# Kernel optimization log

Hardware: AMD Instinct MI355X
Metric: run time of the kernel (lower is better)

The kernel has to match this reference:

```python
import jax, jax.numpy as jnp
import numpy as np

B, S, D = 2, 2048, 1024
H, KV, HD = 16, 4, 64          # heads, kv heads, head_dim = D//H
I, E, K = 3584, 4, 2            # ffn intermediate, routed experts, top_k
WIN = 512                       # sliding window
EPS = 1e-5
THETA = 1000000.0
LIMIT = 7.0                     # swiglu clamp
NREP = H // KV
NEG = -1e30

def _rms(x, w):
    return x * jax.lax.rsqrt(jnp.mean(x * x, axis=-1, keepdims=True) + EPS) * w

def _rot_half(x):
    h = x.shape[-1] // 2
    return jnp.concatenate([-x[..., h:], x[..., :h]], axis=-1)

def _ffn(x, gw, uw, dw):
    g = jnp.minimum(x @ gw.T, LIMIT)
    u = jnp.clip(x @ uw.T, -LIMIT, LIMIT)
    return (jax.nn.silu(g) * u) @ dw.T

def setup_inputs():
    key = jax.random.key(0)
    ks = jax.random.split(key, 16)
    # rotary embeddings [S, HD]
    inv = 1.0 / (THETA ** (jnp.arange(0, HD, 2, dtype=jnp.float32) / HD))
    freqs = jnp.outer(jnp.arange(S, dtype=jnp.float32), inv)
    emb = jnp.concatenate([freqs, freqs], axis=-1)
    s = 0.02
    return dict(
        x=jax.random.normal(ks[0], (B, S, D), jnp.float32),
        cos=jnp.cos(emb), sin=jnp.sin(emb),
        attn_norm_w=jnp.ones((D,), jnp.float32),
        post_norm_w=jnp.ones((D,), jnp.float32),
        q_norm_w=jnp.ones((HD,), jnp.float32),
        k_norm_w=jnp.ones((HD,), jnp.float32),
        wq=jax.random.normal(ks[1], (H * HD, D), jnp.float32) * s,
        wk=jax.random.normal(ks[2], (KV * HD, D), jnp.float32) * s,
        wv=jax.random.normal(ks[3], (KV * HD, D), jnp.float32) * s,
        wo=jax.random.normal(ks[4], (D, H * HD), jnp.float32) * s,
        sinks=jax.random.normal(ks[5], (H,), jnp.float32),
        gate_w=jax.random.normal(ks[6], (E, D), jnp.float32) * s,
        eg_w=jax.random.normal(ks[7], (E, I, D), jnp.float32) * s,
        eu_w=jax.random.normal(ks[8], (E, I, D), jnp.float32) * s,
        ed_w=jax.random.normal(ks[9], (E, D, I), jnp.float32) * s,
        sg_w=jax.random.normal(ks[10], (I, D), jnp.float32) * s,
        su_w=jax.random.normal(ks[11], (I, D), jnp.float32) * s,
        sd_w=jax.random.normal(ks[12], (D, I), jnp.float32) * s,
    )

def _forward(x, cos, sin, attn_norm_w, wq, wk, wv, wo, q_norm_w, k_norm_w,
             sinks, post_norm_w, gate_w, eg_w, eu_w, ed_w, sg_w, su_w, sd_w):
    # ---- attention sublayer ----
    hin = _rms(x, attn_norm_w)
    q = (hin @ wq.T).reshape(B, S, H, HD)
    k = (hin @ wk.T).reshape(B, S, KV, HD)
    v = (hin @ wv.T).reshape(B, S, KV, HD)
    q = _rms(q, q_norm_w)
    k = _rms(k, k_norm_w)
    c, sn = cos[None, :, None, :], sin[None, :, None, :]
    q = q * c + _rot_half(q) * sn
    k = k * c + _rot_half(k) * sn
    k = jnp.repeat(k, NREP, axis=2)  # GQA -> [B,S,H,HD]
    v = jnp.repeat(v, NREP, axis=2)
    scores = jnp.einsum('bihd,bjhd->bhij', q, k) / np.sqrt(HD).astype(np.float32)
    idx = jnp.arange(S)
    allowed = (idx[:, None] >= idx[None, :]) & (idx[None, :] > idx[:, None] - WIN)
    scores = jnp.where(allowed[None, None], scores, NEG)
    sink = jnp.broadcast_to(sinks.reshape(1, H, 1, 1), (B, H, S, 1))
    ext = jnp.concatenate([scores, sink], axis=-1)           # [B,H,S,S+1]
    w = jax.nn.softmax(ext.astype(jnp.float32), axis=-1)[..., :-1].astype(x.dtype)
    attn = jnp.einsum('bhij,bjhd->bihd', w, v).reshape(B, S, H * HD) @ wo.T
    h1 = x + attn
    # ---- MoE FFN sublayer ----
    m = _rms(h1, post_norm_w).reshape(-1, D)                 # [T,D]
    T = m.shape[0]
    gs = jax.nn.softmax(m @ gate_w.T, axis=-1)               # [T,E]
    tw, ti = jax.lax.top_k(gs, K)
    tw = tw / (jnp.sum(tw, axis=-1, keepdims=True) + 1e-20)  # norm_topk_prob
    wd = jnp.zeros((T, E), m.dtype).at[jnp.arange(T)[:, None], ti].add(tw)
    g = jnp.minimum(jnp.einsum('td,eid->tei', m, eg_w), LIMIT)
    u = jnp.clip(jnp.einsum('td,eid->tei', m, eu_w), -LIMIT, LIMIT)
    eo = jnp.einsum('tei,edi->ted', jax.nn.silu(g) * u, ed_w)
    y = jnp.einsum('ted,te->td', eo, wd) + _ffn(m, sg_w, su_w, sd_w)
    return h1 + y.reshape(B, S, D)

def reference(x, cos, sin, attn_norm_w, post_norm_w, q_norm_w, k_norm_w,
              wq, wk, wv, wo, sinks, gate_w, eg_w, eu_w, ed_w, sg_w, su_w, sd_w):
    return _forward(x, cos, sin, attn_norm_w, wq, wk, wv, wo, q_norm_w, k_norm_w,
                    sinks, post_norm_w, gate_w, eg_w, eu_w, ed_w, sg_w, su_w, sd_w)
```

## Files before the change

### kernel.cpp

```cpp
#include <hip/hip_runtime.h>
#include <cstdint>
#include <cstddef>

#define S_LEN 2048
#define BATCH 2
#define DMODEL 1024
#define NH 16
#define NKV 4
#define HDIM 64
#define NTOK 4096
#define IDIM 3584
#define NEXP 4
#define WINSZ 512
#define EPSV 1e-5f
#define LIMV 7.0f
#define CATMAX 13056

typedef unsigned short u16;
typedef unsigned int u32;
typedef __bf16 bf16x8 __attribute__((ext_vector_type(8)));
typedef float f32x4 __attribute__((ext_vector_type(4)));
typedef u32 u32x4 __attribute__((ext_vector_type(4)));
typedef u16 u16x4 __attribute__((ext_vector_type(4)));

__device__ __forceinline__ u16 f2b(float f) {
  union { float f; u32 u; } v; v.f = f;
  return (u16)((v.u + 0x7fffu + ((v.u >> 16) & 1u)) >> 16);
}
__device__ __forceinline__ float b2f(u16 h) {
  union { u32 u; float f; } v; v.u = ((u32)h) << 16; return v.f;
}
__device__ __forceinline__ float wave_sum(float x) {
#pragma unroll
  for (int o = 32; o > 0; o >>= 1) x += __shfl_xor(x, o);
  return x;
}
__device__ __forceinline__ void gld16(const void* g, void* l) {
  __builtin_amdgcn_global_load_lds(
      (const __attribute__((address_space(1))) u32*)g,
      (__attribute__((address_space(3))) u32*)l, 16, 0, 0);
}
__device__ __forceinline__ int xcd_swz(int id, int nwg) {
  int q = nwg >> 3, rr = nwg & 7;
  int xcd = id & 7, j = id >> 3;
  return (xcd < rr ? xcd * (q + 1) : rr * (q + 1) + (xcd - rr) * q) + j;
}

__global__ void k_init(int* cnt) {
  if (threadIdx.x < NEXP) cnt[threadIdx.x] = 0;
}

struct CvtArgs {
  const float* src[10];
  u16* dh[10];
  u16* dl[10];
  int n4[10];
};
__global__ __launch_bounds__(256) void k_convert(CvtArgs a) {
  int ai = blockIdx.y;
  const f32x4* s = (const f32x4*)a.src[ai];
  u16* dh = a.dh[ai];
  u16* dl = a.dl[ai];
  int n4 = a.n4[ai];
  for (int i = blockIdx.x * 256 + threadIdx.x; i < n4; i += gridDim.x * 256) {
    f32x4 v = s[i];
    u16x4 h;
    h.x = f2b(v.x); h.y = f2b(v.y); h.z = f2b(v.z); h.w = f2b(v.w);
    ((u16x4*)dh)[i] = h;
    if (dl) {
      u16x4 lo;
      lo.x = f2b(v.x - b2f(h.x)); lo.y = f2b(v.y - b2f(h.y));
      lo.z = f2b(v.z - b2f(h.z)); lo.w = f2b(v.w - b2f(h.w));
      ((u16x4*)dl)[i] = lo;
    }
  }
}

__global__ __launch_bounds__(256) void k_rms_split(const float* __restrict__ x,
                                                   const float* __restrict__ w,
                                                   u16* __restrict__ oh, u16* __restrict__ ol) {
  int row = blockIdx.x;
  int t = threadIdx.x;
  const f32x4* xr = (const f32x4*)(x + (size_t)row * DMODEL);
  f32x4 v = xr[t];
  float ss = v.x * v.x + v.y * v.y + v.z * v.z + v.w * v.w;
  ss = wave_sum(ss);
  __shared__ float red[4];
  int wid = t >> 6;
  if ((t & 63) == 0) red[wid] = ss;
  __syncthreads();
  float tot = red[0] + red[1] + red[2] + red[3];
  float r = rsqrtf(tot * (1.0f / DMODEL) + EPSV);
  f32x4 wv = ((const f32x4*)w)[t];
  float y0 = v.x * r * wv.x, y1 = v.y * r * wv.y, y2 = v.z * r * wv.z, y3 = v.w * r * wv.w;
  u16x4 h; h.x = f2b(y0); h.y = f2b(y1); h.z = f2b(y2); h.w = f2b(y3);
  u16x4 lo; lo.x = f2b(y0 - b2f(h.x)); lo.y = f2b(y1 - b2f(h.y));
  lo.z = f2b(y2 - b2f(h.z)); lo.w = f2b(y3 - b2f(h.w));
  ((u16x4*)(oh + (size_t)row * DMODEL))[t] = h;
  ((u16x4*)(ol + (size_t)row * DMODEL))[t] = lo;
}

__global__ __launch_bounds__(256) void k_qkprep(const float* __restrict__ qkv,
                                                const float* __restrict__ cosb,
                                                const float* __restrict__ sinb,
                                                const float* __restrict__ qw,
                                                const float* __restrict__ kw,
                                                u16* __restrict__ qhh, u16* __restrict__ qll,
                                                u16* __restrict__ khh, u16* __restrict__ kll,
                                                u16* __restrict__ vhh, u16* __restrict__ vll) {
  int t = blockIdx.x;
  int b = t / S_LEN, s = t - b * S_LEN;
  int wid = threadIdx.x >> 6, l = threadIdx.x & 63;
  const float* row = qkv + (size_t)t * 1536;
  float c = cosb[s * 64 + l], sn = sinb[s * 64 + l];
#pragma unroll
  for (int ii = 0; ii < 6; ii++) {
    int u = wid + 4 * ii;
    if (u < 16) {
      float v = row[u * 64 + l];
      float ss = wave_sum(v * v);
      float r = rsqrtf(ss * (1.0f / 64.0f) + EPSV);
      float vn = v * r * qw[l];
      float p = __shfl_xor(vn, 32);
      float o = (l < 32) ? (vn * c - p * sn) : (vn * c + p * sn);
      o *= 0.125f;
      size_t base = (((size_t)(b * NH + u)) * S_LEN + s) * 64 + l;
      u16 hi = f2b(o);
      qhh[base] = hi; qll[base] = f2b(o - b2f(hi));
    } else if (u < 20) {
      int kv = u - 16;
      float v = row[1024 + kv * 64 + l];
      float ss = wave_sum(v * v);
      float r = rsqrtf(ss * (1.0f / 64.0f) + EPSV);
      float vn = v * r * kw[l];
      float p = __shfl_xor(vn, 32);
      float o = (l < 32) ? (vn * c - p * sn) : (vn * c + p * sn);
      size_t base = (((size_t)(b * NKV + kv)) * S_LEN + s) * 64 + l;
      u16 hi = f2b(o);
      khh[base] = hi; kll[base] = f2b(o - b2f(hi));
    } else {
      int kv = u - 20;
      float v = row[1280 + kv * 64 + l];
      size_t base = (((size_t)(b * NKV + kv)) * S_LEN + s) * 64 + l;
      u16 hi = f2b(v);
      vhh[base] = hi; vll[base] = f2b(v - b2f(hi));
    }
  }
}

__global__ __launch_bounds__(256) void k_vtrans(const u16* __restrict__ vh,
                                                const u16* __restrict__ vl,
                                                u16* __restrict__ vth, u16* __restrict__ vtl) {
  int kb = blockIdx.x;
  int gg = blockIdx.y;
  __shared__ u16 Th[128 * 64], Tl[128 * 64];
  int t = threadIdx.x;
  const u16* sh = vh + (((size_t)gg * S_LEN) + kb * 128) * 64;
  const u16* sl = vl + (((size_t)gg * S_LEN) + kb * 128) * 64;
#pragma unroll
  for (int p = 0; p < 8; p++) {
    int idx = p * 256 + t;
    int key = idx >> 4, dq = idx & 15;
    u16x4 a = *(const u16x4*)(sh + key * 64 + dq * 4);
    u16x4 bb = *(const u16x4*)(sl + key * 64 + dq * 4);
    int off = key * 128 + ((dq * 8) ^ ((key & 7) << 4));
    *(u16x4*)((char*)Th + off) = a;
    *(u16x4*)((char*)Tl + off) = bb;
  }
  __syncthreads();
  int d = t >> 2, kq = t & 3;
  u16 outh[32], outl[32];
#pragma unroll
  for (int jj = 0; jj < 32; jj++) {
    int key = kq * 32 + jj;
    int off = key * 128 + ((d * 2) ^ ((key & 7) << 4));
    outh[jj] = *(const u16*)((const char*)Th + off);
    outl[jj] = *(const u16*)((const char*)Tl + off);
  }
  u16* dsth = vth + (((size_t)gg * 64) + d) * S_LEN + kb * 128 + kq * 32;
  u16* dstl = vtl + (((size_t)gg * 64) + d) * S_LEN + kb * 128 + kq * 32;
#pragma unroll
  for (int q4 = 0; q4 < 8; q4++) {
    u16x4 a = {outh[q4 * 4], outh[q4 * 4 + 1], outh[q4 * 4 + 2], outh[q4 * 4 + 3]};
    u16x4 bb = {outl[q4 * 4], outl[q4 * 4 + 1], outl[q4 * 4 + 2], outl[q4 * 4 + 3]};
    *(u16x4*)(dsth + q4 * 4) = a;
    *(u16x4*)(dstl + q4 * 4) = bb;
  }
}

__global__ __launch_bounds__(256) void k_attn_mfma(
    const u16* __restrict__ qhp, const u16* __restrict__ qlp,
    const u16* __restrict__ khp, const u16* __restrict__ klp,
    const u16* __restrict__ vthp, const u16* __restrict__ vtlp,
    const float* __restrict__ sinks,
    u16* __restrict__ oh, u16* __restrict__ ol) {
  int qt = blockIdx.x;
  int bh = blockIdx.y;
  int h = bh & 15, b = bh >> 4;
  int kvg = b * NKV + (h >> 2);
  int qbase = qt * 64;
  int t = threadIdx.x, w = t >> 6, l = t & 63;
  int g = l >> 4, li = l & 15;

  __shared__ u16 Qh[4096], Ql[4096], Kh[4096], Kl[4096], Vh[4096], Vl[4096];
  __shared__ u16 Ph[4][1024], Pl[4][1024];

  {
    const u16* sh = qhp + (((size_t)bh * S_LEN) + qbase) * 64;
    const u16* sl = qlp + (((size_t)bh * S_LEN) + qbase) * 64;
#pragma unroll
    for (int p = 0; p < 2; p++) {
      int idx = p * 256 + t;
      int row = idx >> 3, seg = idx & 7;
      u32x4 a = *(const u32x4*)(sh + row * 64 + seg * 8);
      u32x4 bb = *(const u32x4*)(sl + row * 64 + seg * 8);
      int off = row * 128 + ((seg * 16) ^ ((row & 7) << 4));
      *(u32x4*)((char*)Qh + off) = a;
      *(u32x4*)((char*)Ql + off) = bb;
    }
  }

  float m_[4], lsum[4];
  f32x4 accv[4];
  float sk = sinks[h];
#pragma unroll
  for (int j = 0; j < 4; j++) { m_[j] = sk; lsum[j] = 1.0f; }
#pragma unroll
  for (int nt = 0; nt < 4; nt++) accv[nt] = (f32x4){0.f, 0.f, 0.f, 0.f};

  int j0s = qbase - WINSZ; if (j0s < 0) j0s = 0;
  const u16* khb = khp + ((size_t)kvg * S_LEN) * 64;
  const u16* klb = klp + ((size_t)kvg * S_LEN) * 64;
  const u16* vthb = vthp + ((size_t)kvg * 64) * S_LEN;
  const u16* vtlb = vtlp + ((size_t)kvg * 64) * S_LEN;

  for (int j0 = j0s; j0 <= qbase; j0 += 64) {
    __syncthreads();
#pragma unroll
    for (int p = 0; p < 2; p++) {
      int idx = p * 256 + t;
      int row = idx >> 3, seg = idx & 7;
      int off = row * 128 + ((seg * 16) ^ ((row & 7) << 4));
      *(u32x4*)((char*)Kh + off) = *(const u32x4*)(khb + ((size_t)(j0 + row)) * 64 + seg * 8);
      *(u32x4*)((char*)Kl + off) = *(const u32x4*)(klb + ((size_t)(j0 + row)) * 64 + seg * 8);
      *(u32x4*)((char*)Vh + off) = *(const u32x4*)(vthb + (size_t)row * S_LEN + j0 + seg * 8);
      *(u32x4*)((char*)Vl + off) = *(const u32x4*)(vtlb + (size_t)row * S_LEN + j0 + seg * 8);
    }
    __syncthreads();

    f32x4 S[4];
#pragma unroll
    for (int nt = 0; nt < 4; nt++) S[nt] = (f32x4){0.f, 0.f, 0.f, 0.f};
#pragma unroll
    for (int ks = 0; ks < 2; ks++) {
      int arow = w * 16 + li;
      int coff = ks * 64 + g * 16;
      int ao = arow * 128 + (coff ^ ((arow & 7) << 4));
      bf16x8 qah = *(const bf16x8*)((char*)Qh + ao);
      bf16x8 qal = *(const bf16x8*)((char*)Ql + ao);
#pragma unroll
      for (int nt = 0; nt < 4; nt++) {
        int brow = nt * 16 + li;
        int bo = brow * 128 + (coff ^ ((brow & 7) << 4));
        bf16x8 kbh = *(const bf16x8*)((char*)Kh + bo);
        bf16x8 kbl = *(const bf16x8*)((char*)Kl + bo);
        S[nt] = __builtin_amdgcn_mfma_f32_16x16x32_bf16(qah, kbh, S[nt], 0, 0, 0);
        S[nt] = __builtin_amdgcn_mfma_f32_16x16x32_bf16(qah, kbl, S[nt], 0, 0, 0);
        S[nt] = __builtin_amdgcn_mfma_f32_16x16x32_bf16(qal, kbh, S[nt], 0, 0, 0);
      }
    }

    float scj[4];
#pragma unroll
    for (int j = 0; j < 4; j++) {
      int q = qbase + w * 16 + g * 4 + j;
      float sv[4];
      float mx = -1e30f;
#pragma unroll
      for (int nt = 0; nt < 4; nt++) {
        int key = j0 + nt * 16 + li;
        bool ok = (key <= q) && (key > q - WINSZ);
        sv[nt] = ok ? S[nt][j] : -1e30f;
        mx = fmaxf(mx, sv[nt]);
      }
#pragma unroll
      for (int o = 1; o < 16; o <<= 1) mx = fmaxf(mx, __shfl_xor(mx, o));
      float mn = fmaxf(m_[j], mx);
      float sc = __expf(m_[j] - mn);
      float ps = 0.f;
      float pv[4];
#pragma unroll
      for (int nt = 0; nt < 4; nt++) { pv[nt] = __expf(sv[nt] - mn); ps += pv[nt]; }
#pragma unroll
      for (int o = 1; o < 16; o <<= 1) ps += __shfl_xor(ps, o);
      lsum[j] = lsum[j] * sc + ps;
      m_[j] = mn;
      scj[j] = sc;
      int prow = g * 4 + j;
#pragma unroll
      for (int nt = 0; nt < 4; nt++) {
        int pb = prow * 128 + ((nt * 32 + li * 2) ^ ((prow & 7) << 4));
        u16 hi = f2b(pv[nt]);
        *(u16*)((char*)Ph[w] + pb) = hi;
        *(u16*)((char*)Pl[w] + pb) = f2b(pv[nt] - b2f(hi));
      }
    }
#pragma unroll
    for (int nt = 0; nt < 4; nt++) {
      f32x4 a = accv[nt];
      a[0] *= scj[0]; a[1] *= scj[1]; a[2] *= scj[2]; a[3] *= scj[3];
      accv[nt] = a;
    }

#pragma unroll
    for (int ks = 0; ks < 2; ks++) {
      int coff = ks * 64 + g * 16;
      int pb = li * 128 + (coff ^ ((li & 7) << 4));
      bf16x8 pah = *(const bf16x8*)((char*)Ph[w] + pb);
      bf16x8 pal = *(const bf16x8*)((char*)Pl[w] + pb);
#pragma unroll
      for (int nt = 0; nt < 4; nt++) {
        int vrow = nt * 16 + li;
        int vo = vrow * 128 + (coff ^ ((vrow & 7) << 4));
        bf16x8 vbh = *(const bf16x8*)((char*)Vh + vo);
        bf16x8 vbl = *(const bf16x8*)((char*)Vl + vo);
        accv[nt] = __builtin_amdgcn_mfma_f32_16x16x32_bf16(pah, vbh, accv[nt], 0, 0, 0);
        accv[nt] = __builtin_amdgcn_mfma_f32_16x16x32_bf16(pah, vbl, accv[nt], 0, 0, 0);
        accv[nt] = __builtin_amdgcn_mfma_f32_16x16x32_bf16(pal, vbh, accv[nt], 0, 0, 0);
      }
    }
  }

  float inv[4];
#pragma unroll
  for (int j = 0; j < 4; j++) inv[j] = 1.0f / lsum[j];
#pragma unroll
  for (int nt = 0; nt < 4; nt++) {
#pragma unroll
    for (int j = 0; j < 4; j++) {
      float o = accv[nt][j] * inv[j];
      int token = b * S_LEN + qbase + w * 16 + g * 4 + j;
      size_t off = (size_t)token * (NH * HDIM) + h * 64 + nt * 16 + li;
      u16 hi = f2b(o);
      oh[off] = hi;
      ol[off] = f2b(o - b2f(hi));
    }
  }
}

__global__ __launch_bounds__(256) void k_routing1(const float* __restrict__ h1,
                                                  const float* __restrict__ pw,
                                                  const float* __restrict__ gw,
                                                  u16* __restrict__ mb,
                                                  float* __restrict__ lgbuf) {
  int row = blockIdx.x;
  int t = threadIdx.x;
  int wid = t >> 6;
  const f32x4* xr = (const f32x4*)(h1 + (size_t)row * DMODEL);
  f32x4 v = xr[t];
  float ss = wave_sum(v.x * v.x + v.y * v.y + v.z * v.z + v.w * v.w);
  __shared__ float red[4];
  __shared__ float redp[4][4];
  if ((t & 63) == 0) red[wid] = ss;
  __syncthreads();
  float tot = red[0] + red[1] + red[2] + red[3];
  float r = rsqrtf(tot * (1.0f / DMODEL) + EPSV);
  f32x4 w4 = ((const f32x4*)pw)[t];
  float m0 = v.x * r * w4.x, m1 = v.y * r * w4.y, m2 = v.z * r * w4.z, m3 = v.w * r * w4.w;
  u16x4 hb; hb.x = f2b(m0); hb.y = f2b(m1); hb.z = f2b(m2); hb.w = f2b(m3);
  ((u16x4*)(mb + (size_t)row * DMODEL))[t] = hb;
#pragma unroll
  for (int e = 0; e < NEXP; e++) {
    f32x4 g4 = ((const f32x4*)(gw + (size_t)e * DMODEL))[t];
    float pe = wave_sum(m0 * g4.x + m1 * g4.y + m2 * g4.z + m3 * g4.w);
    if ((t & 63) == 0) redp[wid][e] = pe;
  }
  __syncthreads();
  if (t < NEXP) {
    float lg = redp[0][t] + redp[1][t] + redp[2][t] + redp[3][t];
    lgbuf[(size_t)row * NEXP + t] = lg;
  }
}

__global__ __launch_bounds__(256) void k_route2(const float* __restrict__ lgbuf,
                                                float* __restrict__ wd,
                                                int* __restrict__ cnt,
                                                int* __restrict__ idxb) {
  __shared__ int lcnt[NEXP], gbase[NEXP];
  int t = threadIdx.x;
  int token = blockIdx.x * 256 + t;
  if (t < NEXP) lcnt[t] = 0;
  __syncthreads();
  f32x4 lgv = ((const f32x4*)lgbuf)[token];
  float lg[4] = {lgv.x, lgv.y, lgv.z, lgv.w};
  int i1 = 0;
#pragma unroll
  for (int e = 1; e < NEXP; e++) if (lg[e] > lg[i1]) i1 = e;
  int i2 = -1;
#pragma unroll
  for (int e = 0; e < NEXP; e++) if (e != i1 && (i2 < 0 || lg[e] > lg[i2])) i2 = e;
  float d = __expf(lg[i2] - lg[i1]);
  float w1 = 1.0f / (1.0f + d);
  float w2 = 1.0f - w1;
  float wrow[4] = {0.f, 0.f, 0.f, 0.f};
  wrow[i1] = w1; wrow[i2] = w2;
  ((f32x4*)wd)[token] = (f32x4){wrow[0], wrow[1], wrow[2], wrow[3]};
  int r1 = atomicAdd(&lcnt[i1], 1);
  int r2 = atomicAdd(&lcnt[i2], 1);
  __syncthreads();
  if (t < NEXP) gbase[t] = atomicAdd(&cnt[t], lcnt[t]);
  __syncthreads();
  idxb[i1 * NTOK + gbase[i1] + r1] = token * 2;
  idxb[i2 * NTOK + gbase[i2] + r2] = token * 2 + 1;
}

__global__ __launch_bounds__(256) void k_route3(const int* __restrict__ cnt,
                                                const int* __restrict__ idxb,
                                                const float* __restrict__ wd,
                                                int* __restrict__ idxcat,
                                                float* __restrict__ wcat,
                                                int* __restrict__ pref) {
  int i = blockIdx.x * 256 + threadIdx.x;
  int c0 = cnt[0], c1 = cnt[1], c2 = cnt[2], c3 = cnt[3];
  int p1 = (c0 + 255) & ~255;
  int p2 = p1 + ((c1 + 255) & ~255);
  int p3 = p2 + ((c2 + 255) & ~255);
  int p4 = p3 + ((c3 + 255) & ~255);
  int p5 = p4 + NTOK;
  if (i == 0) {
    pref[0] = 0; pref[1] = p1; pref[2] = p2; pref[3] = p3; pref[4] = p4; pref[5] = p5;
  }
  if (i >= CATMAX) return;
  if (i >= p5) { idxcat[i] = -1; wcat[i] = 0.f; return; }
  if (i >= p4) {
    idxcat[i] = (i - p4) * 4 + 2;
    wcat[i] = 1.0f;
    return;
  }
  int e, base, cn;
  if (i < p1) { e = 0; base = 0; cn = c0; }
  else if (i < p2) { e = 1; base = p1; cn = c1; }
  else if (i < p3) { e = 2; base = p2; cn = c2; }
  else { e = 3; base = p3; cn = c3; }
  int j = i - base;
  if (j < cn) {
    int entry = idxb[e * NTOK + j];
    idxcat[i] = (entry >> 1) * 4 + (entry & 1);
    wcat[i] = wd[(size_t)(entry >> 1) * NEXP + e];
  } else {
    idxcat[i] = -1;
    wcat[i] = 0.f;
  }
}

__global__ __launch_bounds__(512, 2) void k256gu(
    const u16* __restrict__ A, const u16* __restrict__ B1e,
    const u16* __restrict__ B2e,
    const int* __restrict__ idxcat, const int* __restrict__ pref,
    u16* __restrict__ actout) {
  __shared__ u16 As[2][256 * 64];
  __shared__ u16 Bs[2][128 * 64];
  __shared__ u16 Bus[2][128 * 64];
  int nwg = gridDim.x * gridDim.y;
  int swzid = xcd_swz(blockIdx.y * gridDim.x + blockIdx.x, nwg);
  int tn = swzid % gridDim.x, tm = swzid / gridDim.x;
  int Meff = pref[5];
  int r0 = tm * 256;
  if (r0 >= Meff) return;
  int e = (r0 < pref[1]) ? 0 : (r0 < pref[2]) ? 1 : (r0 < pref[3]) ? 2
          : (r0 < pref[4]) ? 3 : 4;
  const u16* B1 = B1e + (size_t)e * IDIM * DMODEL;
  const u16* B2 = B2e + (size_t)e * IDIM * DMODEL;

  int t = threadIdx.x;
  int w = t >> 6, l = t & 63;
  int wm = w >> 2, wn = w & 3;
  int li = l & 15, lh = l >> 4;

  size_t aOff[4];
  int seg = t & 7;
#pragma unroll
  for (int c = 0; c < 4; c++) {
    int r = c * 64 + (t >> 3);
    int swz = (seg ^ (r & 7)) * 8;
    int en = idxcat[r0 + r];
    int row = (en >= 0) ? (en >> 2) : 0;
    aOff[c] = (size_t)row * DMODEL + swz;
  }
  size_t bOff[2];
#pragma unroll
  for (int c = 0; c < 2; c++) {
    int r = c * 64 + (t >> 3);
    int swz = (seg ^ (r & 7)) * 8;
    bOff[c] = (size_t)(tn * 128 + r) * DMODEL + swz;
  }
  int wlds = w * 1024;

  f32x4 acc[8][2], accU[8][2];
#pragma unroll
  for (int f = 0; f < 8; f++)
#pragma unroll
    for (int cf = 0; cf < 2; cf++) {
      acc[f][cf] = (f32x4){0.f, 0.f, 0.f, 0.f};
      accU[f][cf] = (f32x4){0.f, 0.f, 0.f, 0.f};
    }

  auto stage = [&](int buf, int k0) {
    char* ab = (char*)As[buf];
#pragma unroll
    for (int c = 0; c < 4; c++) gld16(A + aOff[c] + k0, ab + c * 8192 + wlds);
    char* bb = (char*)Bs[buf];
#pragma unroll
    for (int c = 0; c < 2; c++) gld16(B1 + bOff[c] + k0, bb + c * 8192 + wlds);
    char* ub = (char*)Bus[buf];
#pragma unroll
    for (int c = 0; c < 2; c++) gld16(B2 + bOff[c] + k0, ub + c * 8192 + wlds);
  };

  stage(0, 0);
  __syncthreads();

  int NT = DMODEL >> 6;
  int cur = 0;
  for (int kt = 0; kt < NT; kt++) {
    if (kt + 1 < NT) stage(cur ^ 1, (kt + 1) << 6);
#pragma unroll
    for (int kk = 0; kk < 2; kk++) {
      bf16x8 af[8];
#pragma unroll
      for (int f = 0; f < 8; f++) {
        int r = wm * 128 + f * 16 + li;
        af[f] = *(const bf16x8*)((const char*)As[cur] + r * 128 +
                                 (((kk * 4 + lh) ^ (r & 7)) << 4));
      }
      bf16x8 bfr[2];
#pragma unroll
      for (int cf = 0; cf < 2; cf++) {
        int r = wn * 32 + cf * 16 + li;
        bfr[cf] = *(const bf16x8*)((const char*)Bs[cur] + r * 128 +
                                   (((kk * 4 + lh) ^ (r & 7)) << 4));
      }
#pragma unroll
      for (int f = 0; f < 8; f++)
#pragma unroll
        for (int cf = 0; cf < 2; cf++)
          acc[f][cf] = __builtin_amdgcn_mfma_f32_16x16x32_bf16(af[f], bfr[cf], acc[f][cf], 0, 0, 0);
      bf16x8 bu[2];
#pragma unroll
      for (int cf = 0; cf < 2; cf++) {
        int r = wn * 32 + cf * 16 + li;
        bu[cf] = *(const bf16x8*)((const char*)Bus[cur] + r * 128 +
                                  (((kk * 4 + lh) ^ (r & 7)) << 4));
      }
#pragma unroll
      for (int f = 0; f < 8; f++)
#pragma unroll
        for (int cf = 0; cf < 2; cf++)
          accU[f][cf] = __builtin_amdgcn_mfma_f32_16x16x32_bf16(af[f], bu[cf], accU[f][cf], 0, 0, 0);
    }
    __syncthreads();
    cur ^= 1;
  }

#pragma unroll
  for (int f = 0; f < 8; f++) {
#pragma unroll
    for (int j = 0; j < 4; j++) {
      int r = r0 + wm * 128 + f * 16 + lh * 4 + j;
#pragma unroll
      for (int cf = 0; cf < 2; cf++) {
        int c = tn * 128 + wn * 32 + cf * 16 + li;
        float g = acc[f][cf][j];
        float u = accU[f][cf][j];
        float gm = fminf(g, LIMV);
        float um = fminf(fmaxf(u, -LIMV), LIMV);
        float a = gm / (1.0f + __expf(-gm)) * um;
        actout[(size_t)r * IDIM + c] = f2b(a);
      }
    }
  }
}

__global__ __launch_bounds__(512, 4) void k256d(
    const u16* __restrict__ A, const u16* __restrict__ B1e,
    const int* __restrict__ idxcat, const float* __restrict__ wcat,
    const int* __restrict__ pref,
    u16* __restrict__ y3) {
  __shared__ u16 As[2][256 * 32];
  __shared__ u16 B1s[2][128 * 32];
  int nwg = gridDim.x * gridDim.y;
  int swzid = xcd_swz(blockIdx.y * gridDim.x + blockIdx.x, nwg);
  int tn = swzid % gridDim.x, tm = swzid / gridDim.x;
  int Meff = pref[5];
  int r0 = tm * 256;
  if (r0 >= Meff) return;
  int e = (r0 < pref[1]) ? 0 : (r0 < pref[2]) ? 1 : (r0 < pref[3]) ? 2
          : (r0 < pref[4]) ? 3 : 4;
  const u16* B1 = B1e + (size_t)e * DMODEL * IDIM;

  int t = threadIdx.x;
  int w = t >> 6, l = t & 63;
  int wm = w >> 2, wn = w & 3;
  int li = l & 15, lh = l >> 4;

  int g = (l & 7) ^ (l >> 3);
  int kchunk = g & 3;
  size_t aG[2];
#pragma unroll
  for (int c = 0; c < 2; c++) {
    int rA = c * 64 + w * 8 + (l >> 3) + 128 * (g >> 2);
    aG[c] = (size_t)(r0 + rA) * IDIM + kchunk * 8;
  }
  size_t bG;
  {
    int rB = w * 8 + (l >> 3) + 64 * (g >> 2);
    bG = (size_t)(tn * 128 + rB) * IDIM + kchunk * 8;
  }
  int wlds = w * 1024;

  int abase = li * 128 + (((wm * 4 + lh) ^ (li & 7)) << 4);
  int bbase = ((wn & 1) * 32 + li) * 128 + ((((wn >> 1) * 4 + lh) ^ (li & 7)) << 4);

  f32x4 acc[8][2];
#pragma unroll
  for (int f = 0; f < 8; f++)
#pragma unroll
    for (int cf = 0; cf < 2; cf++) acc[f][cf] = (f32x4){0.f, 0.f, 0.f, 0.f};

  auto stage = [&](int buf, int k0) {
    char* as = (char*)As[buf];
    gld16(A + aG[0] + k0, as + wlds);
    gld16(A + aG[1] + k0, as + 8192 + wlds);
    gld16(B1 + bG + k0, (char*)B1s[buf] + wlds);
  };

  stage(0, 0);
  __syncthreads();

  int NT = IDIM >> 5;
  int cur = 0;
  for (int kt = 0; kt < NT; kt++) {
    if (kt + 1 < NT) stage(cur ^ 1, (kt + 1) << 5);
    bf16x8 af[8];
#pragma unroll
    for (int f = 0; f < 8; f++)
      af[f] = *(const bf16x8*)((const char*)As[cur] + abase + f * 2048);
    bf16x8 b1f[2];
#pragma unroll
    for (int cf = 0; cf < 2; cf++)
      b1f[cf] = *(const bf16x8*)((const char*)B1s[cur] + bbase + cf * 2048);
#pragma unroll
    for (int f = 0; f < 8; f++)
#pragma unroll
      for (int cf = 0; cf < 2; cf++)
        acc[f][cf] = __builtin_amdgcn_mfma_f32_16x16x32_bf16(af[f], b1f[cf], acc[f][cf], 0, 0, 0);
    __syncthreads();
    cur ^= 1;
  }

#pragma unroll
  for (int f = 0; f < 8; f++) {
#pragma unroll
    for (int j = 0; j < 4; j++) {
      int r = r0 + wm * 128 + f * 16 + lh * 4 + j;
#pragma unroll
      for (int cf = 0; cf < 2; cf++) {
        int c = tn * 128 + wn * 32 + cf * 16 + li;
        int entry = idxcat[r];
        if (entry >= 0) {
          int tok = entry >> 2, slot = entry & 3;
          y3[((size_t)slot * NTOK + tok) * DMODEL + c] = f2b(wcat[r] * acc[f][cf][j]);
        }
      }
    }
  }
}

constexpr int EPI_STORE = 0;
constexpr int EPI_H1 = 1;

template <int EPI>
__global__ __launch_bounds__(256, 2) void k_gemm(
    const u16* __restrict__ Ah, const u16* __restrict__ Al,
    const u16* __restrict__ Bh, const u16* __restrict__ Bl,
    int M, int N, int K, int lda, int ldb,
    float* __restrict__ outF, int ldc, int col0,
    const float* __restrict__ addsrc) {
  __shared__ u16 As[2][2 * 128 * 32];
  __shared__ u16 Bs[2][2 * 128 * 32];
  int tm = blockIdx.y, tn = blockIdx.x;
  int t = threadIdx.x;
  int w = t >> 6, l = t & 63;
  int wr = w >> 1, wc = w & 1;

  size_t a0 = (size_t)(tm * 128 + (t >> 2)) * lda + (t & 3) * 8;
  size_t a1 = a0 + (size_t)64 * lda;
  size_t b0 = (size_t)(tn * 128 + (t >> 2)) * ldb + (t & 3) * 8;
  size_t b1 = b0 + (size_t)64 * ldb;

  f32x4 acc[4][4];
#pragma unroll
  for (int i = 0; i < 4; i++)
#pragma unroll
    for (int j = 0; j < 4; j++) acc[i][j] = (f32x4){0.f, 0.f, 0.f, 0.f};

  int arow = wr * 64 + (l & 15);
  int brow = wc * 64 + (l & 15);
  int koff = (l >> 4) * 8;

  auto stage = [&](int buf, int k0) {
    char* AsW0 = (char*)As[buf] + w * 1024;
    char* AsW1 = (char*)As[buf] + 4096 + w * 1024;
    char* BsW0 = (char*)Bs[buf] + w * 1024;
    char* BsW1 = (char*)Bs[buf] + 4096 + w * 1024;
    gld16(Ah + a0 + k0, AsW0);
    gld16(Ah + a1 + k0, AsW1);
    gld16(Bh + b0 + k0, BsW0);
    gld16(Bh + b1 + k0, BsW1);
    gld16(Al + a0 + k0, AsW0 + 8192);
    gld16(Al + a1 + k0, AsW1 + 8192);
    gld16(Bl + b0 + k0, BsW0 + 8192);
    gld16(Bl + b1 + k0, BsW1 + 8192);
  };

  stage(0, 0);
  __syncthreads();

  int NT = K >> 5;
  int cur = 0;
  for (int kt = 0; kt < NT; kt++) {
    if (kt + 1 < NT) stage(cur ^ 1, (kt + 1) << 5);
    const u16* Asb = As[cur];
    const u16* Bsb = Bs[cur];
    bf16x8 af[2][4], bf[2][4];
#pragma unroll
    for (int mm = 0; mm < 4; mm++) {
      af[0][mm] = *(const bf16x8*)&Asb[(arow + mm * 16) * 32 + koff];
      bf[0][mm] = *(const bf16x8*)&Bsb[(brow + mm * 16) * 32 + koff];
      af[1][mm] = *(const bf16x8*)&Asb[128 * 32 + (arow + mm * 16) * 32 + koff];
      bf[1][mm] = *(const bf16x8*)&Bsb[128 * 32 + (brow + mm * 16) * 32 + koff];
    }
#pragma unroll
    for (int mi = 0; mi < 4; mi++)
#pragma unroll
      for (int ni = 0; ni < 4; ni++) {
        acc[mi][ni] = __builtin_amdgcn_mfma_f32_16x16x32_bf16(af[0][mi], bf[0][ni], acc[mi][ni], 0, 0, 0);
        acc[mi][ni] = __builtin_amdgcn_mfma_f32_16x16x32_bf16(af[0][mi], bf[1][ni], acc[mi][ni], 0, 0, 0);
        acc[mi][ni] = __builtin_amdgcn_mfma_f32_16x16x32_bf16(af[1][mi], bf[0][ni], acc[mi][ni], 0, 0, 0);
      }
    __syncthreads();
    cur ^= 1;
  }

  int rb = tm * 128 + wr * 64 + ((l >> 4) << 2);
  int cb = tn * 128 + wc * 64 + (l & 15);
#pragma unroll
  for (int mi = 0; mi < 4; mi++) {
#pragma unroll
    for (int j = 0; j < 4; j++) {
      int r = rb + mi * 16 + j;
#pragma unroll
      for (int ni = 0; ni < 4; ni++) {
        int c = cb + ni * 16;
        float v = acc[mi][ni][j];
        if constexpr (EPI == EPI_STORE) {
          outF[(size_t)r * ldc + col0 + c] = v;
        } else {
          size_t o = (size_t)r * ldc + c;
          outF[o] = v + addsrc[o];
        }
      }
    }
  }
}

__global__ __launch_bounds__(256) void k_final(const float* __restrict__ h1,
                                               const u16* __restrict__ y3,
                                               float* __restrict__ out) {
  int i = blockIdx.x * 256 + threadIdx.x;
  f32x4 a = ((const f32x4*)h1)[i];
  u16x4 s0 = ((const u16x4*)y3)[i];
  u16x4 s1 = ((const u16x4*)(y3 + (size_t)NTOK * DMODEL))[i];
  u16x4 s2 = ((const u16x4*)(y3 + (size_t)2 * NTOK * DMODEL))[i];
  f32x4 r = {a.x + b2f(s0.x) + b2f(s1.x) + b2f(s2.x),
             a.y + b2f(s0.y) + b2f(s1.y) + b2f(s2.y),
             a.z + b2f(s0.z) + b2f(s1.z) + b2f(s2.z),
             a.w + b2f(s0.w) + b2f(s1.w) + b2f(s2.w)};
  ((f32x4*)out)[i] = r;
}

extern "C" void kernel_launch(void* const* d_in, const int* in_sizes, int n_in,
                              void* d_out, int out_size, void* d_ws, size_t ws_size,
                              hipStream_t stream) {
  (void)in_sizes; (void)n_in; (void)out_size; (void)ws_size;
  const float* x = (const float*)d_in[0];
  const float* cosb = (const float*)d_in[1];
  const float* sinb = (const float*)d_in[2];
  const float* anw = (const float*)d_in[3];
  const float* pnw = (const float*)d_in[4];
  const float* qnw = (const float*)d_in[5];
  const float* knw = (const float*)d_in[6];
  const float* wq = (const float*)d_in[7];
  const float* wk = (const float*)d_in[8];
  const float* wv = (const float*)d_in[9];
  const float* wo = (const float*)d_in[10];
  const float* sinks = (const float*)d_in[11];
  const float* gw = (const float*)d_in[12];
  const float* egw = (const float*)d_in[13];
  const float* euw = (const float*)d_in[14];
  const float* edw = (const float*)d_in[15];
  const float* sgw = (const float*)d_in[16];
  const float* suw = (const float*)d_in[17];
  const float* sdw = (const float*)d_in[18];
  float* out = (float*)d_out;

  char* ws = (char*)d_ws;
  size_t off = 0;
  auto alloc = [&](size_t bytes) -> char* {
    char* p = ws + off;
    off += (bytes + 255) & ~(size_t)255;
    return p;
  };
  const size_t EW = (size_t)IDIM * DMODEL;
  u16* wqkvh = (u16*)alloc((size_t)1536 * 1024 * 2);
  u16* wqkvl = (u16*)alloc((size_t)1536 * 1024 * 2);
  u16* woh = (u16*)alloc(1048576 * 2); u16* wol = (u16*)alloc(1048576 * 2);
  u16* egb5 = (u16*)alloc(5 * EW * 2);
  u16* eub5 = (u16*)alloc(5 * EW * 2);
  u16* edb5 = (u16*)alloc(5 * EW * 2);
  float* h1 = (float*)alloc((size_t)NTOK * DMODEL * 4);
  u16* mb = (u16*)alloc((size_t)NTOK * DMODEL * 2);
  u16* y3 = (u16*)alloc((size_t)3 * NTOK * DMODEL * 2);
  float* wdbuf = (float*)alloc((size_t)NTOK * NEXP * 4);
  float* lgbuf = (float*)alloc((size_t)NTOK * NEXP * 4);
  int* cnt = (int*)alloc(256);
  int* idxb = (int*)alloc((size_t)NEXP * NTOK * 4);
  int* idxcat = (int*)alloc((size_t)CATMAX * 4);
  float* wcat = (float*)alloc((size_t)CATMAX * 4);
  int* pref = (int*)alloc(256);
  char* regA = alloc((size_t)CATMAX * IDIM * 2);
  float* qkvb = (float*)regA;
  u16* qh_ = (u16*)(regA + 25165824);
  u16* ql_ = (u16*)(regA + 33554432);
  u16* kh_ = (u16*)(regA + 41943040);
  u16* kl_ = (u16*)(regA + 44040192);
  u16* vh_ = (u16*)(regA + 46137344);
  u16* vl_ = (u16*)(regA + 48234496);
  u16* vth_ = (u16*)(regA + 50331648);
  u16* vtl_ = (u16*)(regA + 52428800);
  u16* hinh = (u16*)(regA + 54525952);
  u16* hinl = (u16*)(regA + 62914560);
  u16* attnh = (u16*)(regA + 71303168);
  u16* attnl = (u16*)(regA + 79691776);
  u16* actcat = (u16*)regA;

  k_init<<<1, 64, 0, stream>>>(cnt);

  CvtArgs ca;
  const float* srcs[10] = {wq, wk, wv, wo, egw, euw, edw, sgw, suw, sdw};
  u16* dhs[10] = {wqkvh, wqkvh + 1048576, wqkvh + 1310720, woh,
                  egb5, eub5, edb5, egb5 + 4 * EW, eub5 + 4 * EW, edb5 + 4 * EW};
  u16* dls[10] = {wqkvl, wqkvl + 1048576, wqkvl + 1310720, wol,
                  nullptr, nullptr, nullptr, nullptr, nullptr, nullptr};
  int ns[10] = {1048576, 262144, 262144, 1048576, 14680064, 14680064, 14680064,
                3670016, 3670016, 3670016};
  for (int i = 0; i < 10; i++) {
    ca.src[i] = srcs[i]; ca.dh[i] = dhs[i]; ca.dl[i] = dls[i]; ca.n4[i] = ns[i] / 4;
  }
  k_convert<<<dim3(2048, 10), 256, 0, stream>>>(ca);

  k_rms_split<<<NTOK, 256, 0, stream>>>(x, anw, hinh, hinl);

  k_gemm<EPI_STORE><<<dim3(12, 32), 256, 0, stream>>>(
      hinh, hinl, wqkvh, wqkvl, NTOK, 1536, 1024, 1024, 1024,
      qkvb, 1536, 0, nullptr);

  k_qkprep<<<NTOK, 256, 0, stream>>>(qkvb, cosb, sinb, qnw, knw,
                                     qh_, ql_, kh_, kl_, vh_, vl_);
  k_vtrans<<<dim3(16, 8), 256, 0, stream>>>(vh_, vl_, vth_, vtl_);
  k_attn_mfma<<<dim3(32, 32), 256, 0, stream>>>(qh_, ql_, kh_, kl_, vth_, vtl_,
                                                sinks, attnh, attnl);

  k_gemm<EPI_H1><<<dim3(8, 32), 256, 0, stream>>>(
      attnh, attnl, woh, wol, NTOK, 1024, 1024, 1024, 1024,
      h1, 1024, 0, x);

  k_routing1<<<NTOK, 256, 0, stream>>>(h1, pnw, gw, mb, lgbuf);
  k_route2<<<16, 256, 0, stream>>>(lgbuf, wdbuf, cnt, idxb);
  k_route3<<<CATMAX / 256, 256, 0, stream>>>(cnt, idxb, wdbuf, idxcat, wcat, pref);

  k256gu<<<dim3(IDIM / 128, CATMAX / 256), 512, 0, stream>>>(
      mb, egb5, eub5, idxcat, pref, actcat);
  k256d<<<dim3(DMODEL / 128, CATMAX / 256), 512, 0, stream>>>(
      actcat, edb5, idxcat, wcat, pref, y3);

  k_final<<<4096, 256, 0, stream>>>(h1, y3, out);
}
```

Before: 620.6 us.

## Split fused gate/up MoE GEMM into two lighter passes with higher occupancy

```diff
diff --git a/kernel.cpp b/kernel.cpp
--- a/kernel.cpp
+++ b/kernel.cpp
@@ -453,14 +453,13 @@
   }
 }
 
-__global__ __launch_bounds__(512, 2) void k256gu(
-    const u16* __restrict__ A, const u16* __restrict__ B1e,
-    const u16* __restrict__ B2e,
+template <int PH>
+__global__ __launch_bounds__(512, 4) void k256p(
+    const u16* __restrict__ A, const u16* __restrict__ Be,
     const int* __restrict__ idxcat, const int* __restrict__ pref,
     u16* __restrict__ actout) {
-  __shared__ u16 As[2][256 * 64];
-  __shared__ u16 Bs[2][128 * 64];
-  __shared__ u16 Bus[2][128 * 64];
+  __shared__ u16 As[2][256 * 32];
+  __shared__ u16 B1s[2][128 * 32];
   int nwg = gridDim.x * gridDim.y;
   int swzid = xcd_swz(blockIdx.y * gridDim.x + blockIdx.x, nwg);
   int tn = swzid % gridDim.x, tm = swzid / gridDim.x;
@@ -469,95 +468,66 @@
   if (r0 >= Meff) return;
   int e = (r0 < pref[1]) ? 0 : (r0 < pref[2]) ? 1 : (r0 < pref[3]) ? 2
           : (r0 < pref[4]) ? 3 : 4;
-  const u16* B1 = B1e + (size_t)e * IDIM * DMODEL;
-  const u16* B2 = B2e + (size_t)e * IDIM * DMODEL;
+  const u16* B1 = Be + (size_t)e * IDIM * DMODEL;
 
   int t = threadIdx.x;
   int w = t >> 6, l = t & 63;
   int wm = w >> 2, wn = w & 3;
   int li = l & 15, lh = l >> 4;
 
-  size_t aOff[4];
-  int seg = t & 7;
-#pragma unroll
-  for (int c = 0; c < 4; c++) {
-    int r = c * 64 + (t >> 3);
-    int swz = (seg ^ (r & 7)) * 8;
-    int en = idxcat[r0 + r];
+  int g = (l & 7) ^ (l >> 3);
+  int kchunk = g & 3;
+  size_t aG[2];
+#pragma unroll
+  for (int c = 0; c < 2; c++) {
+    int rA = c * 64 + w * 8 + (l >> 3) + 128 * (g >> 2);
+    int en = idxcat[r0 + rA];
     int row = (en >= 0) ? (en >> 2) : 0;
-    aOff[c] = (size_t)row * DMODEL + swz;
-  }
-  size_t bOff[2];
-#pragma unroll
-  for (int c = 0; c < 2; c++) {
-    int r = c * 64 + (t >> 3);
-    int swz = (seg ^ (r & 7)) * 8;
-    bOff[c] = (size_t)(tn * 128 + r) * DMODEL + swz;
+    aG[c] = (size_t)row * DMODEL + kchunk * 8;
+  }
+  size_t bG;
+  {
+    int rB = w * 8 + (l >> 3) + 64 * (g >> 2);
+    bG = (size_t)(tn * 128 + rB) * DMODEL + kchunk * 8;
   }
   int wlds = w * 1024;
 
-  f32x4 acc[8][2], accU[8][2];
+  int abase = li * 128 + (((wm * 4 + lh) ^ (li & 7)) << 4);
+  int bbase = ((wn & 1) * 32 + li) * 128 + ((((wn >> 1) * 4 + lh) ^ (li & 7)) << 4);
+
+  f32x4 acc[8][2];
 #pragma unroll
   for (int f = 0; f < 8; f++)
 #pragma unroll
-    for (int cf = 0; cf < 2; cf++) {
-      acc[f][cf] = (f32x4){0.f, 0.f, 0.f, 0.f};
-      accU[f][cf] = (f32x4){0.f, 0.f, 0.f, 0.f};
-    }
+    for (int cf = 0; cf < 2; cf++) acc[f][cf] = (f32x4){0.f, 0.f, 0.f, 0.f};
 
   auto stage = [&](int buf, int k0) {
-    char* ab = (char*)As[buf];
-#pragma unroll
-    for (int c = 0; c < 4; c++) gld16(A + aOff[c] + k0, ab + c * 8192 + wlds);
-    char* bb = (char*)Bs[buf];
-#pragma unroll
-    for (int c = 0; c < 2; c++) gld16(B1 + bOff[c] + k0, bb + c * 8192 + wlds);
-    char* ub = (char*)Bus[buf];
-#pragma unroll
-    for (int c = 0; c < 2; c++) gld16(B2 + bOff[c] + k0, ub + c * 8192 + wlds);
+    char* as = (char*)As[buf];
+    gld16(A + aG[0] + k0, as + wlds);
+    gld16(A + aG[1] + k0, as + 8192 + wlds);
+    gld16(B1 + bG + k0, (char*)B1s[buf] + wlds);
   };
 
   stage(0, 0);
   __syncthreads();
 
-  int NT = DMODEL >> 6;
+  int NT = DMODEL >> 5;
   int cur = 0;
   for (int kt = 0; kt < NT; kt++) {
-    if (kt + 1 < NT) stage(cur ^ 1, (kt + 1) << 6);
-#pragma unroll
-    for (int kk = 0; kk < 2; kk++) {
-      bf16x8 af[8];
-#pragma unroll
-      for (int f = 0; f < 8; f++) {
-        int r = wm * 128 + f * 16 + li;
-        af[f] = *(const bf16x8*)((const char*)As[cur] + r * 128 +
-                                 (((kk * 4 + lh) ^ (r & 7)) << 4));
-      }
-      bf16x8 bfr[2];
-#pragma unroll
-      for (int cf = 0; cf < 2; cf++) {
-        int r = wn * 32 + cf * 16 + li;
-        bfr[cf] = *(const bf16x8*)((const char*)Bs[cur] + r * 128 +
-                                   (((kk * 4 + lh) ^ (r & 7)) << 4));
-      }
-#pragma unroll
-      for (int f = 0; f < 8; f++)
-#pragma unroll
-        for (int cf = 0; cf < 2; cf++)
-          acc[f][cf] = __builtin_amdgcn_mfma_f32_16x16x32_bf16(af[f], bfr[cf], acc[f][cf], 0, 0, 0);
-      bf16x8 bu[2];
-#pragma unroll
-      for (int cf = 0; cf < 2; cf++) {
-        int r = wn * 32 + cf * 16 + li;
-        bu[cf] = *(const bf16x8*)((const char*)Bus[cur] + r * 128 +
-                                  (((kk * 4 + lh) ^ (r & 7)) << 4));
-      }
-#pragma unroll
-      for (int f = 0; f < 8; f++)
-#pragma unroll
-        for (int cf = 0; cf < 2; cf++)
-          accU[f][cf] = __builtin_amdgcn_mfma_f32_16x16x32_bf16(af[f], bu[cf], accU[f][cf], 0, 0, 0);
-    }
+    if (kt + 1 < NT) stage(cur ^ 1, (kt + 1) << 5);
+    bf16x8 af[8];
+#pragma unroll
+    for (int f = 0; f < 8; f++)
+      af[f] = *(const bf16x8*)((const char*)As[cur] + abase + f * 2048);
+    bf16x8 b1f[2];
+#pragma unroll
+    for (int cf = 0; cf < 2; cf++)
+      b1f[cf] = *(const bf16x8*)((const char*)B1s[cur] + bbase + cf * 2048);
+#pragma unroll
+    for (int f = 0; f < 8; f++)
+#pragma unroll
+      for (int cf = 0; cf < 2; cf++)
+        acc[f][cf] = __builtin_amdgcn_mfma_f32_16x16x32_bf16(af[f], b1f[cf], acc[f][cf], 0, 0, 0);
     __syncthreads();
     cur ^= 1;
   }
@@ -570,12 +540,16 @@
 #pragma unroll
       for (int cf = 0; cf < 2; cf++) {
         int c = tn * 128 + wn * 32 + cf * 16 + li;
-        float g = acc[f][cf][j];
-        float u = accU[f][cf][j];
-        float gm = fminf(g, LIMV);
-        float um = fminf(fmaxf(u, -LIMV), LIMV);
-        float a = gm / (1.0f + __expf(-gm)) * um;
-        actout[(size_t)r * IDIM + c] = f2b(a);
+        size_t o = (size_t)r * IDIM + c;
+        float v = acc[f][cf][j];
+        if constexpr (PH == 0) {
+          actout[o] = f2b(fminf(v, LIMV));
+        } else {
+          float gm = b2f(actout[o]);
+          float um = fminf(fmaxf(v, -LIMV), LIMV);
+          float a = gm / (1.0f + __expf(-gm)) * um;
+          actout[o] = f2b(a);
+        }
       }
     }
   }
@@ -889,8 +863,10 @@
   k_route2<<<16, 256, 0, stream>>>(lgbuf, wdbuf, cnt, idxb);
   k_route3<<<CATMAX / 256, 256, 0, stream>>>(cnt, idxb, wdbuf, idxcat, wcat, pref);
 
-  k256gu<<<dim3(IDIM / 128, CATMAX / 256), 512, 0, stream>>>(
-      mb, egb5, eub5, idxcat, pref, actcat);
+  k256p<0><<<dim3(IDIM / 128, CATMAX / 256), 512, 0, stream>>>(
+      mb, egb5, idxcat, pref, actcat);
+  k256p<1><<<dim3(IDIM / 128, CATMAX / 256), 512, 0, stream>>>(
+      mb, eub5, idxcat, pref, actcat);
   k256d<<<dim3(DMODEL / 128, CATMAX / 256), 512, 0, stream>>>(
       actcat, edb5, idxcat, wcat, pref, y3);
 
```

Result: slower. 649.9 us (+4.7%).
